# Performance work log

Hardware: AMD Instinct MI355X
Metric: run time of the kernel (lower is better)

## Reference

```python
import jax, jax.numpy as jnp
import numpy as np
import math

N = 10000      # num nodes
DEG = 3        # base avg out-degree of random directed graph
D = 128        # d_model
H = 8          # heads
C = D // H     # head dim
L = 2          # num_layers
HOPS = 2       # num_hops


def _build_attn_window(rng):
    # random directed base graph
    E0 = N * DEG
    s0 = rng.integers(0, N, E0).astype(np.int64)
    d0 = rng.integers(0, N, E0).astype(np.int64)
    # to_undirected + coalesce
    s = np.concatenate([s0, d0]); d = np.concatenate([d0, s0])
    key = np.unique(s * N + d)
    s, d = key // N, key % N
    # add self loops (as in _get_attn_window) and coalesce
    loops = np.arange(N, dtype=np.int64)
    key = np.unique(np.concatenate([loops * N + loops, s * N + d]))
    s, d = key // N, key % N
    # base adjacency in CSR-like form grouped by source
    order = np.argsort(s, kind='stable')
    bss, bsd = s[order], d[order]
    outdeg = np.bincount(bss, minlength=N)
    indptr = np.concatenate([[0], np.cumsum(outdeg)])
    # k_hop = A; for _ in range(HOPS-1): k_hop = k_hop @ A   (boolean sparse product)
    cs, cd = s.copy(), d.copy()
    for _ in range(HOPS - 1):
        counts = outdeg[cd]
        total = int(counts.sum())
        new_s = np.repeat(cs, counts)
        starts = np.repeat(indptr[cd], counts)
        offs = np.arange(total, dtype=np.int64) - np.repeat(
            np.concatenate([[0], np.cumsum(counts)])[:-1], counts)
        new_d = bsd[starts + offs]
        key = np.unique(new_s * N + new_d)
        cs, cd = key // N, key % N
    return np.stack([cs, cd]).astype(np.int64)  # [2, E2] (src, dst)


def setup_inputs() -> dict:
    rng = np.random.default_rng(0)
    aw = _build_attn_window(rng)
    key = jax.random.key(0)
    ks = jax.random.split(key, 10)
    sc = 1.0 / math.sqrt(D)
    x = jax.random.normal(ks[0], (N, D), jnp.float32)
    Wq = jax.random.normal(ks[1], (L, D, D), jnp.float32) * sc
    Wk = jax.random.normal(ks[2], (L, D, D), jnp.float32) * sc
    Wv = jax.random.normal(ks[3], (L, D, D), jnp.float32) * sc
    Ws = jax.random.normal(ks[4], (L, D, D), jnp.float32) * sc
    bq = jax.random.normal(ks[5], (L, D), jnp.float32) * 0.01
    bk = jax.random.normal(ks[6], (L, D), jnp.float32) * 0.01
    bv = jax.random.normal(ks[7], (L, D), jnp.float32) * 0.01
    bs = jax.random.normal(ks[8], (L, D), jnp.float32) * 0.01
    return {"x": x, "Wq": Wq, "bq": bq, "Wk": Wk, "bk": bk,
            "Wv": Wv, "bv": bv, "Ws": Ws, "bs": bs,
            "attn_window": jnp.asarray(aw)}


def _segment_softmax(logits, seg):
    # logits: [E, H], seg: [E] destination node ids (every node has a self loop)
    m = jax.ops.segment_max(logits, seg, num_segments=N)
    e = jnp.exp(logits - m[seg])
    z = jax.ops.segment_sum(e, seg, num_segments=N)
    return e / z[seg]


def _transformer_conv(h, wq, bq_, wk, bk_, wv, bv_, ws, bs_, src, dst):
    # PyG TransformerConv (concat=True, root_weight=True, beta=False, eval mode)
    q = (h @ wq + bq_).reshape(N, H, C)
    k = (h @ wk + bk_).reshape(N, H, C)
    v = (h @ wv + bv_).reshape(N, H, C)
    logits = jnp.einsum('ehc,ehc->eh', q[dst], k[src]) * (1.0 / math.sqrt(C))
    alpha = _segment_softmax(logits, dst)                       # [E, H]
    agg = jax.ops.segment_sum(alpha[:, :, None] * v[src], dst,  # [N, H, C]
                              num_segments=N)
    return agg.reshape(N, D) + h @ ws + bs_


def reference(x, Wq, bq, Wk, bk, Wv, bv, Ws, bs, attn_window):
    src, dst = attn_window[0], attn_window[1]
    h = x
    for l in range(L - 1):
        h = jax.nn.relu(h + _transformer_conv(
            h, Wq[l], bq[l], Wk[l], bk[l], Wv[l], bv[l], Ws[l], bs[l], src, dst))
    l = L - 1
    h = h + _transformer_conv(
        h, Wq[l], bq[l], Wk[l], bk[l], Wv[l], bv[l], Ws[l], bs[l], src, dst)
    return h
```

## Files before the change

kernel.cpp:

```cpp
#include <hip/hip_runtime.h>
#include <hip/hip_bf16.h>

typedef __hip_bfloat16 bf16;
typedef __attribute__((ext_vector_type(8))) short bf16x8v;
typedef __attribute__((ext_vector_type(4))) float f32x4v;

#define N_NODES 10000
#define DMODEL  128
#define NHEADS  8
#define CHEAD   16


__device__ __forceinline__ float bf2f(unsigned u) {
    union { unsigned i; float f; } c; c.i = u << 16; return c.f;
}
__device__ __forceinline__ unsigned short f2bf_bits(float f) {
    bf16 b = __float2bfloat16(f);
    return *(unsigned short*)&b;
}

__global__ void build_csr(const int* __restrict__ aw, int E,
                          int* __restrict__ rowptr, int* __restrict__ nbr,
                          const float* __restrict__ x,
                          unsigned short* __restrict__ xb) {
    __shared__ int nz;
    if (threadIdx.x == 0) nz = 0;
    __syncthreads();
    int W = 4096;
    if (W > 2 * E) W = 2 * E;
    int any = 0;
    for (int w = 1 + 2 * (int)threadIdx.x; w < W; w += 2 * blockDim.x)
        any |= aw[w];
    if (any) atomicOr(&nz, 1);
    __syncthreads();
    const int is64 = (nz == 0);

    const int gid = blockIdx.x * blockDim.x + threadIdx.x;
    const int gtotal = gridDim.x * blockDim.x;

    for (int i = gid; i < N_NODES * DMODEL / 8; i += gtotal) {
        float4 a = *(const float4*)&x[i * 8];
        float4 b = *(const float4*)&x[i * 8 + 4];
        uint4 u;
        u.x = f2bf_bits(a.x) | ((unsigned)f2bf_bits(a.y) << 16);
        u.y = f2bf_bits(a.z) | ((unsigned)f2bf_bits(a.w) << 16);
        u.z = f2bf_bits(b.x) | ((unsigned)f2bf_bits(b.y) << 16);
        u.w = f2bf_bits(b.z) | ((unsigned)f2bf_bits(b.w) << 16);
        *(uint4*)&xb[i * 8] = u;
    }

    int e = gid;
    if (e == 0) rowptr[N_NODES] = E;
    if (e < E) {
        int s  = is64 ? aw[2 * e] : aw[e];
        if (s < 0) s = 0;
        if (s >= N_NODES) s = N_NODES - 1;
        int sp = (e == 0) ? -1 : (is64 ? aw[2 * (e - 1)] : aw[e - 1]);
        for (int r = sp + 1; r <= s; ++r) rowptr[r] = e;
        if (e == E - 1)
            for (int r = s + 1; r < N_NODES; ++r) rowptr[r] = E;
        int d = is64 ? aw[2 * (E + e)] : aw[E + e];
        if (d < 0) d = 0;
        if (d >= N_NODES) d = N_NODES - 1;
        nbr[e] = d;
    }
}

__global__ __launch_bounds__(256) void gemm_qkvs(
    const unsigned short* __restrict__ A,
    const float* __restrict__ Wq, const float* __restrict__ Wk,
    const float* __restrict__ Wv, const float* __restrict__ Ws,
    const float* __restrict__ bq, const float* __restrict__ bk,
    const float* __restrict__ bv, const float* __restrict__ bs,
    int welem, int belem,
    float* __restrict__ qo, bf16* __restrict__ ko, bf16* __restrict__ vo,
    float* __restrict__ hso)
{
    const int cb    = blockIdx.x;
    const int row0  = blockIdx.y * 64;
    const int col0g = cb * 64;
    const int mat   = col0g >> 7;
    const float* W    = (mat == 0) ? Wq : (mat == 1) ? Wk : (mat == 2) ? Wv : Ws;
    const float* bias = (mat == 0) ? bq : (mat == 1) ? bk : (mat == 2) ? bv : bs;
    const int colW0 = col0g & 127;

    __shared__ unsigned short As[64][136];
    __shared__ unsigned short Bs[128][68];

    const int tid = threadIdx.x;

    #pragma unroll
    for (int i = 0; i < 4; ++i) {
        int idx = tid + i * 256;
        int row = idx >> 4, k8 = idx & 15;
        int grow = row0 + row;
        uint4 u = make_uint4(0u, 0u, 0u, 0u);
        if (grow < N_NODES)
            u = *(const uint4*)&A[grow * DMODEL + k8 * 8];
        *(uint4*)&As[row][k8 * 8] = u;
    }
    #pragma unroll
    for (int i = 0; i < 8; ++i) {
        int idx = tid + i * 256;
        int kk = idx >> 4, n4 = idx & 15;
        float4 wv = *(const float4*)&W[welem + kk * DMODEL + colW0 + n4 * 4];
        ushort4 p;
        p.x = f2bf_bits(wv.x); p.y = f2bf_bits(wv.y);
        p.z = f2bf_bits(wv.z); p.w = f2bf_bits(wv.w);
        *(ushort4*)&Bs[kk][n4 * 4] = p;
    }
    __syncthreads();

    const int wave = tid >> 6, lane = tid & 63;
    const int ln = lane & 15, quad = lane >> 4;
    const int ncol = wave * 16 + ln;

    f32x4v acc[4];
    #pragma unroll
    for (int mt = 0; mt < 4; ++mt) acc[mt] = (f32x4v){0.f, 0.f, 0.f, 0.f};

    #pragma unroll
    for (int ks = 0; ks < 4; ++ks) {
        const int kb = ks * 32 + quad * 8;
        bf16x8v bfv;
        #pragma unroll
        for (int j = 0; j < 8; ++j) bfv[j] = (short)Bs[kb + j][ncol];
        #pragma unroll
        for (int mt = 0; mt < 4; ++mt) {
            bf16x8v afv = *(const bf16x8v*)&As[mt * 16 + ln][kb];
            acc[mt] = __builtin_amdgcn_mfma_f32_16x16x32_bf16(afv, bfv,
                                                              acc[mt], 0, 0, 0);
        }
    }

    const float bcol = bias[belem + colW0 + ncol];
    #pragma unroll
    for (int mt = 0; mt < 4; ++mt) {
        #pragma unroll
        for (int r = 0; r < 4; ++r) {
            int row = row0 + mt * 16 + quad * 4 + r;
            if (row >= N_NODES) continue;
            float val = acc[mt][r] + bcol;
            int elo = row * DMODEL + colW0 + ncol;
            if (mat == 0)      qo[elo] = val;
            else if (mat == 3) hso[elo] = val;
            else if (mat == 1) ko[elo] = __float2bfloat16(val);
            else               vo[elo] = __float2bfloat16(val);
        }
    }
}

__global__ __launch_bounds__(256) void attn_fused(
    const float* __restrict__ q, const bf16* __restrict__ k,
    const bf16* __restrict__ v, const float* __restrict__ hs,
    const float* __restrict__ hin,
    const int* __restrict__ rowptr, const int* __restrict__ nbr,
    float* __restrict__ out, unsigned short* __restrict__ outb,
    int relu_flag)
{
    const int wavesPerBlock = blockDim.x >> 6;
    const int wid = blockIdx.x * wavesPerBlock + (threadIdx.x >> 6);
    const int nWaves = gridDim.x * wavesPerBlock;
    const int l = threadIdx.x & 63;
    const int h = l & 7, slot = l >> 3;
    const int hc = l >> 3;

    for (int d = wid; d < N_NODES; d += nWaves) {
        float qf[16];
        const float* qp = q + d * DMODEL + h * CHEAD;
        #pragma unroll
        for (int i = 0; i < 4; ++i) {
            float4 t4 = *(const float4*)(qp + i * 4);
            qf[i * 4 + 0] = t4.x; qf[i * 4 + 1] = t4.y;
            qf[i * 4 + 2] = t4.z; qf[i * 4 + 3] = t4.w;
        }

        const int e0 = rowptr[d], e1 = rowptr[d + 1];
        float m_run = -3.0e38f, zacc = 0.f;
        float2 acc = make_float2(0.f, 0.f);

        int eg = e0 + slot;
        bool pad_cur = !(eg < e1);
        int s_cur = pad_cur ? d : nbr[eg];
        const uint4* kp0 = (const uint4*)(k + s_cur * DMODEL + h * CHEAD);
        uint4 kc0 = kp0[0], kc1 = kp0[1];

        for (int base = e0; base < e1; base += 8) {
            int en = base + 8 + slot;
            bool pad_nxt = !(en < e1);
            int s_nxt = pad_nxt ? d : nbr[en];
            const uint4* kpn = (const uint4*)(k + s_nxt * DMODEL + h * CHEAD);
            uint4 kn0 = kpn[0], kn1 = kpn[1];

            int se[8];
            #pragma unroll
            for (int e = 0; e < 8; ++e) se[e] = __shfl(s_cur, e * 8);
            unsigned uv[8];
            #pragma unroll
            for (int e = 0; e < 8; ++e)
                uv[e] = *(const unsigned*)(v + se[e] * DMODEL + 2 * l);

            const unsigned* w0 = (const unsigned*)&kc0;
            const unsigned* w1 = (const unsigned*)&kc1;
            float dot = 0.f;
            #pragma unroll
            for (int w = 0; w < 4; ++w) {
                dot += qf[w * 2 + 0] * bf2f(w0[w] & 0xffffu);
                dot += qf[w * 2 + 1] * bf2f(w0[w] >> 16);
            }
            #pragma unroll
            for (int w = 0; w < 4; ++w) {
                dot += qf[8 + w * 2 + 0] * bf2f(w1[w] & 0xffffu);
                dot += qf[8 + w * 2 + 1] * bf2f(w1[w] >> 16);
            }
            float p = pad_cur ? -3.0e38f : dot * 0.25f;

            float gm = p;
            gm = fmaxf(gm, __shfl_xor(gm, 8));
            gm = fmaxf(gm, __shfl_xor(gm, 16));
            gm = fmaxf(gm, __shfl_xor(gm, 32));
            float mnew = fmaxf(m_run, gm);
            float scale = __expf(m_run - mnew);
            m_run = mnew;
            float pe = __expf(p - mnew);
            zacc = zacc * scale + pe;

            float scB = __shfl(scale, hc);
            acc.x *= scB; acc.y *= scB;
            float pee[8];
            #pragma unroll
            for (int e = 0; e < 8; ++e) pee[e] = __shfl(pe, e * 8 + hc);
            #pragma unroll
            for (int e = 0; e < 8; ++e) {
                acc.x += pee[e] * bf2f(uv[e] & 0xffffu);
                acc.y += pee[e] * bf2f(uv[e] >> 16);
            }

            kc0 = kn0; kc1 = kn1; s_cur = s_nxt; pad_cur = pad_nxt;
        }

        float z = zacc;
        z += __shfl_xor(z, 8);
        z += __shfl_xor(z, 16);
        z += __shfl_xor(z, 32);
        float zh = __shfl(z, hc);
        float inv = (zh > 0.f) ? (1.f / zh) : 0.f;

        int idx = d * DMODEL + 2 * l;
        float2 hsv = *(const float2*)(hs + idx);
        float2 hiv = *(const float2*)(hin + idx);
        float2 o;
        o.x = acc.x * inv + hsv.x + hiv.x;
        o.y = acc.y * inv + hsv.y + hiv.y;
        if (relu_flag) { o.x = fmaxf(o.x, 0.f); o.y = fmaxf(o.y, 0.f); }
        *(float2*)(out + idx) = o;
        if (outb) {
            unsigned pk = f2bf_bits(o.x) | ((unsigned)f2bf_bits(o.y) << 16);
            *(unsigned*)&outb[idx] = pk;
        }
    }
}

extern "C" void kernel_launch(void* const* d_in, const int* in_sizes, int n_in,
                              void* d_out, int out_size, void* d_ws, size_t ws_size,
                              hipStream_t stream) {
    const float* x  = (const float*)d_in[0];
    const float* Wq = (const float*)d_in[1];
    const float* bq = (const float*)d_in[2];
    const float* Wk = (const float*)d_in[3];
    const float* bk = (const float*)d_in[4];
    const float* Wv = (const float*)d_in[5];
    const float* bv = (const float*)d_in[6];
    const float* Ws = (const float*)d_in[7];
    const float* bs = (const float*)d_in[8];
    const int*   aw = (const int*)d_in[9];
    const int E = in_sizes[9] / 2;

    char* ws = (char*)d_ws;
    size_t off = 0;
    float* qb = (float*)(ws + off);  off += (size_t)N_NODES * DMODEL * 4;
    bf16*  kb = (bf16*)(ws + off);   off += (size_t)N_NODES * DMODEL * 2;
    bf16*  vb = (bf16*)(ws + off);   off += (size_t)N_NODES * DMODEL * 2;
    float* hsb = (float*)(ws + off); off += (size_t)N_NODES * DMODEL * 4;
    float* h1 = (float*)(ws + off);  off += (size_t)N_NODES * DMODEL * 4;
    unsigned short* xbb = (unsigned short*)(ws + off);
    off += (size_t)N_NODES * DMODEL * 2;
    unsigned short* h1b = (unsigned short*)(ws + off);
    off += (size_t)N_NODES * DMODEL * 2;
    int* rowptr = (int*)(ws + off);  off += ((size_t)N_NODES + 2) * 4;
    int* nbr    = (int*)(ws + off);  off += (size_t)E * 4;

    int cblocks = (E + 255) / 256;
    const int convBlocks = (N_NODES * DMODEL / 8 + 255) / 256;
    if (cblocks < convBlocks) cblocks = convBlocks;
    build_csr<<<cblocks, 256, 0, stream>>>(aw, E, rowptr, nbr, x, xbb);

    dim3 ggrid(8, (N_NODES + 63) / 64);
    const int ablocks = (N_NODES + 3) / 4;

    gemm_qkvs<<<ggrid, 256, 0, stream>>>(xbb, Wq, Wk, Wv, Ws, bq, bk, bv, bs,
                                         0, 0, qb, kb, vb, hsb);
    attn_fused<<<ablocks, 256, 0, stream>>>(qb, kb, vb, hsb, x, rowptr, nbr,
                                            h1, h1b, 1);
    gemm_qkvs<<<ggrid, 256, 0, stream>>>(h1b, Wq, Wk, Wv, Ws, bq, bk, bv, bs,
                                         DMODEL * DMODEL, DMODEL,
                                         qb, kb, vb, hsb);
    attn_fused<<<ablocks, 256, 0, stream>>>(qb, kb, vb, hsb, h1, rowptr, nbr,
                                            (float*)d_out, (unsigned short*)0, 0);
}
```

Measured before the change: 165.6 us.

## Fuse all phases into one persistent kernel with software grid barriers

Merges the CSR build, both QKVS GEMMs and both attention passes into a single persistent kernel sized to occupancy. Phases are separated by an atomic-counter grid barrier instead of separate launches. The goal is to remove four kernel launch gaps and tail effects. It adds barrier spin cost, per-call host occupancy queries and a memset, lower occupancy from the launch_bounds(256,2) limit, and a deadlock risk if not all blocks are co-resident.

```diff
diff --git a/kernel.cpp b/kernel.cpp
--- a/kernel.cpp
+++ b/kernel.cpp
@@ -9,6 +9,7 @@
 #define DMODEL  128
 #define NHEADS  8
 #define CHEAD   16
+#define NRB     ((N_NODES + 63) / 64)
 
 
 __device__ __forceinline__ float bf2f(unsigned u) {
@@ -19,21 +20,41 @@
     return *(unsigned short*)&b;
 }
 
-__global__ void build_csr(const int* __restrict__ aw, int E,
-                          int* __restrict__ rowptr, int* __restrict__ nbr,
-                          const float* __restrict__ x,
-                          unsigned short* __restrict__ xb) {
-    __shared__ int nz;
-    if (threadIdx.x == 0) nz = 0;
+__device__ __forceinline__ void gbar(int* cnt, int* gen, int nb) {
+    __syncthreads();
+    if (threadIdx.x == 0) {
+        __threadfence();
+        int g = atomicAdd(gen, 0);
+        int prev = atomicAdd(cnt, 1);
+        if (prev == nb - 1) {
+            atomicExch(cnt, 0);
+            __threadfence();
+            atomicAdd(gen, 1);
+        } else {
+            while (atomicAdd(gen, 0) == g)
+                __builtin_amdgcn_s_sleep(2);
+        }
+        __threadfence();
+    }
+    __syncthreads();
+}
+
+__device__ __forceinline__ void csr_phase(
+    const int* __restrict__ aw, int E,
+    int* __restrict__ rowptr, int* __restrict__ nbr,
+    const float* __restrict__ x, unsigned short* __restrict__ xb,
+    int* nzp)
+{
+    if (threadIdx.x == 0) *nzp = 0;
     __syncthreads();
     int W = 4096;
     if (W > 2 * E) W = 2 * E;
     int any = 0;
     for (int w = 1 + 2 * (int)threadIdx.x; w < W; w += 2 * blockDim.x)
         any |= aw[w];
-    if (any) atomicOr(&nz, 1);
+    if (any) atomicOr(nzp, 1);
     __syncthreads();
-    const int is64 = (nz == 0);
+    const int is64 = (*nzp == 0);
 
     const int gid = blockIdx.x * blockDim.x + threadIdx.x;
     const int gtotal = gridDim.x * blockDim.x;
@@ -49,9 +70,8 @@
         *(uint4*)&xb[i * 8] = u;
     }
 
-    int e = gid;
-    if (e == 0) rowptr[N_NODES] = E;
-    if (e < E) {
+    if (gid == 0) rowptr[N_NODES] = E;
+    for (int e = gid; e < E; e += gtotal) {
         int s  = is64 ? aw[2 * e] : aw[e];
         if (s < 0) s = 0;
         if (s >= N_NODES) s = N_NODES - 1;
@@ -66,7 +86,7 @@
     }
 }
 
-__global__ __launch_bounds__(256) void gemm_qkvs(
+__device__ __forceinline__ void gemm_phase(
     const unsigned short* __restrict__ A,
     const float* __restrict__ Wq, const float* __restrict__ Wk,
     const float* __restrict__ Wv, const float* __restrict__ Ws,
@@ -74,83 +94,85 @@
     const float* __restrict__ bv, const float* __restrict__ bs,
     int welem, int belem,
     float* __restrict__ qo, bf16* __restrict__ ko, bf16* __restrict__ vo,
-    float* __restrict__ hso)
+    float* __restrict__ hso,
+    unsigned short (*As)[136], unsigned short (*Bs)[68])
 {
-    const int cb    = blockIdx.x;
-    const int row0  = blockIdx.y * 64;
-    const int col0g = cb * 64;
-    const int mat   = col0g >> 7;
-    const float* W    = (mat == 0) ? Wq : (mat == 1) ? Wk : (mat == 2) ? Wv : Ws;
-    const float* bias = (mat == 0) ? bq : (mat == 1) ? bk : (mat == 2) ? bv : bs;
-    const int colW0 = col0g & 127;
-
-    __shared__ unsigned short As[64][136];
-    __shared__ unsigned short Bs[128][68];
-
     const int tid = threadIdx.x;
-
-    #pragma unroll
-    for (int i = 0; i < 4; ++i) {
-        int idx = tid + i * 256;
-        int row = idx >> 4, k8 = idx & 15;
-        int grow = row0 + row;
-        uint4 u = make_uint4(0u, 0u, 0u, 0u);
-        if (grow < N_NODES)
-            u = *(const uint4*)&A[grow * DMODEL + k8 * 8];
-        *(uint4*)&As[row][k8 * 8] = u;
-    }
-    #pragma unroll
-    for (int i = 0; i < 8; ++i) {
-        int idx = tid + i * 256;
-        int kk = idx >> 4, n4 = idx & 15;
-        float4 wv = *(const float4*)&W[welem + kk * DMODEL + colW0 + n4 * 4];
-        ushort4 p;
-        p.x = f2bf_bits(wv.x); p.y = f2bf_bits(wv.y);
-        p.z = f2bf_bits(wv.z); p.w = f2bf_bits(wv.w);
-        *(ushort4*)&Bs[kk][n4 * 4] = p;
-    }
-    __syncthreads();
-
-    const int wave = tid >> 6, lane = tid & 63;
-    const int ln = lane & 15, quad = lane >> 4;
-    const int ncol = wave * 16 + ln;
-
-    f32x4v acc[4];
-    #pragma unroll
-    for (int mt = 0; mt < 4; ++mt) acc[mt] = (f32x4v){0.f, 0.f, 0.f, 0.f};
-
-    #pragma unroll
-    for (int ks = 0; ks < 4; ++ks) {
-        const int kb = ks * 32 + quad * 8;
-        bf16x8v bfv;
-        #pragma unroll
-        for (int j = 0; j < 8; ++j) bfv[j] = (short)Bs[kb + j][ncol];
+    for (int tile = blockIdx.x; tile < 8 * NRB; tile += gridDim.x) {
+        const int cb   = tile & 7;
+        const int row0 = (tile >> 3) * 64;
+        const int mat  = cb >> 1;
+        const float* W    = (mat == 0) ? Wq : (mat == 1) ? Wk
+                          : (mat == 2) ? Wv : Ws;
+        const float* bias = (mat == 0) ? bq : (mat == 1) ? bk
+                          : (mat == 2) ? bv : bs;
+        const int colW0 = (cb & 1) * 64;
+
+        __syncthreads();
+        #pragma unroll
+        for (int i = 0; i < 4; ++i) {
+            int idx = tid + i * 256;
+            int row = idx >> 4, k8 = idx & 15;
+            int grow = row0 + row;
+            uint4 u = make_uint4(0u, 0u, 0u, 0u);
+            if (grow < N_NODES)
+                u = *(const uint4*)&A[grow * DMODEL + k8 * 8];
+            *(uint4*)&As[row][k8 * 8] = u;
+        }
+        #pragma unroll
+        for (int i = 0; i < 8; ++i) {
+            int idx = tid + i * 256;
+            int kk = idx >> 4, n4 = idx & 15;
+            float4 wv = *(const float4*)&W[welem + kk * DMODEL
+                                           + colW0 + n4 * 4];
+            ushort4 p;
+            p.x = f2bf_bits(wv.x); p.y = f2bf_bits(wv.y);
+            p.z = f2bf_bits(wv.z); p.w = f2bf_bits(wv.w);
+            *(ushort4*)&Bs[kk][n4 * 4] = p;
+        }
+        __syncthreads();
+
+        const int wave = tid >> 6, lane = tid & 63;
+        const int ln = lane & 15, quad = lane >> 4;
+        const int ncol = wave * 16 + ln;
+
+        f32x4v acc[4];
+        #pragma unroll
+        for (int mt = 0; mt < 4; ++mt) acc[mt] = (f32x4v){0.f, 0.f, 0.f, 0.f};
+
+        #pragma unroll
+        for (int ks = 0; ks < 4; ++ks) {
+            const int kb = ks * 32 + quad * 8;
+            bf16x8v bfv;
+            #pragma unroll
+            for (int j = 0; j < 8; ++j) bfv[j] = (short)Bs[kb + j][ncol];
+            #pragma unroll
+            for (int mt = 0; mt < 4; ++mt) {
+                bf16x8v afv = *(const bf16x8v*)&As[mt * 16 + ln][kb];
+                acc[mt] = __builtin_amdgcn_mfma_f32_16x16x32_bf16(
+                    afv, bfv, acc[mt], 0, 0, 0);
+            }
+        }
+
+        const float bcol = bias[belem + colW0 + ncol];
         #pragma unroll
         for (int mt = 0; mt < 4; ++mt) {
-            bf16x8v afv = *(const bf16x8v*)&As[mt * 16 + ln][kb];
-            acc[mt] = __builtin_amdgcn_mfma_f32_16x16x32_bf16(afv, bfv,
-                                                              acc[mt], 0, 0, 0);
-        }
-    }
-
-    const float bcol = bias[belem + colW0 + ncol];
-    #pragma unroll
-    for (int mt = 0; mt < 4; ++mt) {
-        #pragma unroll
-        for (int r = 0; r < 4; ++r) {
-            int row = row0 + mt * 16 + quad * 4 + r;
-            if (row >= N_NODES) continue;
-            float val = acc[mt][r] + bcol;
-            int elo = row * DMODEL + colW0 + ncol;
-            if (mat == 0)      qo[elo] = val;
-            else if (mat == 3) hso[elo] = val;
-            else if (mat == 1) ko[elo] = __float2bfloat16(val);
-            else               vo[elo] = __float2bfloat16(val);
-        }
-    }
-}
-
-__global__ __launch_bounds__(256) void attn_fused(
+            #pragma unroll
+            for (int r = 0; r < 4; ++r) {
+                int row = row0 + mt * 16 + quad * 4 + r;
+                if (row >= N_NODES) continue;
+                float val = acc[mt][r] + bcol;
+                int elo = row * DMODEL + colW0 + ncol;
+                if (mat == 0)      qo[elo] = val;
+                else if (mat == 3) hso[elo] = val;
+                else if (mat == 1) ko[elo] = __float2bfloat16(val);
+                else               vo[elo] = __float2bfloat16(val);
+            }
+        }
+    }
+}
+
+__device__ __forceinline__ void attn_phase(
     const float* __restrict__ q, const bf16* __restrict__ k,
     const bf16* __restrict__ v, const float* __restrict__ hs,
     const float* __restrict__ hin,
@@ -158,9 +180,8 @@
     float* __restrict__ out, unsigned short* __restrict__ outb,
     int relu_flag)
 {
-    const int wavesPerBlock = blockDim.x >> 6;
-    const int wid = blockIdx.x * wavesPerBlock + (threadIdx.x >> 6);
-    const int nWaves = gridDim.x * wavesPerBlock;
+    const int wid = blockIdx.x * 4 + (threadIdx.x >> 6);
+    const int nWaves = gridDim.x * 4;
     const int l = threadIdx.x & 63;
     const int h = l & 7, slot = l >> 3;
     const int hc = l >> 3;
@@ -259,6 +280,42 @@
             *(unsigned*)&outb[idx] = pk;
         }
     }
+}
+
+__global__ __launch_bounds__(256, 2) void fused_all(
+    const int* __restrict__ aw, int E,
+    const float* __restrict__ x,
+    const float* __restrict__ Wq, const float* __restrict__ bq,
+    const float* __restrict__ Wk, const float* __restrict__ bk,
+    const float* __restrict__ Wv, const float* __restrict__ bv,
+    const float* __restrict__ Ws, const float* __restrict__ bs,
+    float* __restrict__ qb, bf16* __restrict__ kb, bf16* __restrict__ vb,
+    float* __restrict__ hsb, float* __restrict__ h1,
+    unsigned short* __restrict__ xbb, unsigned short* __restrict__ h1b,
+    int* __restrict__ rowptr, int* __restrict__ nbr,
+    int* __restrict__ bar,
+    float* __restrict__ out)
+{
+    __shared__ unsigned short As[64][136];
+    __shared__ unsigned short Bs[128][68];
+    __shared__ int nz;
+    const int nb = gridDim.x;
+
+    csr_phase(aw, E, rowptr, nbr, x, xbb, &nz);
+    gbar(bar, bar + 1, nb);
+
+    gemm_phase(xbb, Wq, Wk, Wv, Ws, bq, bk, bv, bs, 0, 0,
+               qb, kb, vb, hsb, As, Bs);
+    gbar(bar, bar + 1, nb);
+
+    attn_phase(qb, kb, vb, hsb, x, rowptr, nbr, h1, h1b, 1);
+    gbar(bar, bar + 1, nb);
+
+    gemm_phase(h1b, Wq, Wk, Wv, Ws, bq, bk, bv, bs,
+               DMODEL * DMODEL, DMODEL, qb, kb, vb, hsb, As, Bs);
+    gbar(bar, bar + 1, nb);
+
+    attn_phase(qb, kb, vb, hsb, h1, rowptr, nbr, out, (unsigned short*)0, 0);
 }
 
 extern "C" void kernel_launch(void* const* d_in, const int* in_sizes, int n_in,
@@ -274,7 +331,7 @@
     const float* Ws = (const float*)d_in[7];
     const float* bs = (const float*)d_in[8];
     const int*   aw = (const int*)d_in[9];
-    const int E = in_sizes[9] / 2;
+    int E = in_sizes[9] / 2;
 
     char* ws = (char*)d_ws;
     size_t off = 0;
@@ -289,22 +346,23 @@
     off += (size_t)N_NODES * DMODEL * 2;
     int* rowptr = (int*)(ws + off);  off += ((size_t)N_NODES + 2) * 4;
     int* nbr    = (int*)(ws + off);  off += (size_t)E * 4;
-
-    int cblocks = (E + 255) / 256;
-    const int convBlocks = (N_NODES * DMODEL / 8 + 255) / 256;
-    if (cblocks < convBlocks) cblocks = convBlocks;
-    build_csr<<<cblocks, 256, 0, stream>>>(aw, E, rowptr, nbr, x, xbb);
-
-    dim3 ggrid(8, (N_NODES + 63) / 64);
-    const int ablocks = (N_NODES + 3) / 4;
-
-    gemm_qkvs<<<ggrid, 256, 0, stream>>>(xbb, Wq, Wk, Wv, Ws, bq, bk, bv, bs,
-                                         0, 0, qb, kb, vb, hsb);
-    attn_fused<<<ablocks, 256, 0, stream>>>(qb, kb, vb, hsb, x, rowptr, nbr,
-                                            h1, h1b, 1);
-    gemm_qkvs<<<ggrid, 256, 0, stream>>>(h1b, Wq, Wk, Wv, Ws, bq, bk, bv, bs,
-                                         DMODEL * DMODEL, DMODEL,
-                                         qb, kb, vb, hsb);
-    attn_fused<<<ablocks, 256, 0, stream>>>(qb, kb, vb, hsb, h1, rowptr, nbr,
-                                            (float*)d_out, (unsigned short*)0, 0);
-}
+    int* bar    = (int*)(ws + off);  off += 64;
+
+    hipMemsetAsync(bar, 0, 2 * sizeof(int), stream);
+
+    int dev = 0;
+    hipGetDevice(&dev);
+    int nCU = 0;
+    hipDeviceGetAttribute(&nCU, hipDeviceAttributeMultiprocessorCount, dev);
+    if (nCU <= 0) nCU = 256;
+    int maxB = 0;
+    hipOccupancyMaxActiveBlocksPerMultiprocessor(&maxB,
+        (const void*)fused_all, 256, 0);
+    if (maxB <= 0) maxB = 1;
+    int grid = nCU * maxB;
+
+    float* outp = (float*)d_out;
+    fused_all<<<grid, 256, 0, stream>>>(
+        aw, E, x, Wq, bq, Wk, bk, Wv, bv, Ws, bs,
+        qb, kb, vb, hsb, h1, xbb, h1b, rowptr, nbr, bar, outp);
+}
```

Result: slower. 445.5 us (+169.0%).
